# Kernel optimization log

Hardware: AMD Instinct MI355X
Metric: run time of the kernel (lower is better)

Reference implementation:

```python
import jax, jax.numpy as jnp
import numpy as np
from jax.ops import segment_sum

N_NODES = 50000


def graph_conv(src, dst, x, W, b, n_nodes):
    # DGL GraphConv with norm='both' (allow_zero_in_degree=True):
    # h = D_in^{-1/2} * A^T (D_out^{-1/2} * x) W + b, degrees clamped to >=1
    ones = jnp.ones(src.shape[0], dtype=x.dtype)
    deg_out = jnp.clip(segment_sum(ones, src, num_segments=n_nodes), 1.0)
    deg_in = jnp.clip(segment_sum(ones, dst, num_segments=n_nodes), 1.0)
    h = x * jax.lax.rsqrt(deg_out)[:, None]
    h = h @ W                      # apply weight before aggregation (mult_W first)
    m = segment_sum(h[src], dst, num_segments=n_nodes)  # sparse neighbor sum
    return m * jax.lax.rsqrt(deg_in)[:, None] + b


def setup_inputs() -> dict:
    key = jax.random.key(0)
    ks = jax.random.split(key, 10)
    n, e = N_NODES, 1600000
    d_in, h1, h2, h3 = 128, 128, 128, 64
    in_feat = jax.random.normal(ks[0], (n, d_in), dtype=jnp.float32)
    src = jax.random.randint(ks[1], (e,), 0, n, dtype=jnp.int32)
    dst = jax.random.randint(ks[2], (e,), 0, n, dtype=jnp.int32)
    s = lambda fi, fo: (1.0 / np.sqrt(fi)).astype(np.float32)
    W1 = jax.random.normal(ks[3], (d_in, h1), dtype=jnp.float32) * s(d_in, h1)
    b1 = jnp.zeros((h1,), dtype=jnp.float32)
    W2 = jax.random.normal(ks[4], (h1, h2), dtype=jnp.float32) * s(h1, h2)
    b2 = jnp.zeros((h2,), dtype=jnp.float32)
    Wf = jax.random.normal(ks[5], (h2, h3), dtype=jnp.float32) * s(h2, h3)
    bf = jnp.zeros((h3,), dtype=jnp.float32)
    return {"in_feat": in_feat, "src": src, "dst": dst,
            "W1": W1, "b1": b1, "W2": W2, "b2": b2, "Wf": Wf, "bf": bf}


def reference(in_feat, src, dst, W1, b1, W2, b2, Wf, bf):
    n = in_feat.shape[0]
    h = graph_conv(src, dst, in_feat, W1, b1, n)
    h = jax.nn.relu(h)
    # dropout(p=0.2) is identity in eval mode
    h = graph_conv(src, dst, h, W2, b2, n)
    return h @ Wf + bf
```

## Files before the change

### kernel.cpp

```cpp
#include <hip/hip_runtime.h>
#include <hip/hip_fp16.h>

#define FD 128
#define OD 64
#define RN 256
#define CHUNKS 256
#define NRMAX 1024

typedef _Float16 f16x8 __attribute__((ext_vector_type(8)));
typedef float    f32x4 __attribute__((ext_vector_type(4)));
typedef float    f32x2 __attribute__((ext_vector_type(2)));


__global__ void prescale_kernel(const float* __restrict__ X, const float* __restrict__ r_out,
                                __half* __restrict__ Xs, int n4) {
    int i = blockIdx.x * 256 + threadIdx.x;
    if (i >= n4) return;
    int v = i >> 5;
    float r = r_out[v];
    float4 t = ((const float4*)X)[i];
    ((__half2*)Xs)[2 * i]     = __floats2half2_rn(t.x * r, t.y * r);
    ((__half2*)Xs)[2 * i + 1] = __floats2half2_rn(t.z * r, t.w * r);
}


__global__ __launch_bounds__(1024) void region_hist_kernel(const int* __restrict__ src,
                                                           const int* __restrict__ dst,
                                                           int* __restrict__ hist_g,
                                                           int* __restrict__ hist_gs,
                                                           int E, int NR, int CS) {
    __shared__ int hist[NRMAX];
    __shared__ int hist_s[NRMAX];
    int c = blockIdx.x;
    for (int t = threadIdx.x; t < NR; t += 1024) { hist[t] = 0; hist_s[t] = 0; }
    __syncthreads();
    int e0 = c * CS, e1 = min(e0 + CS, E);
    int nv = (e1 - e0) & ~3;
    for (int e = e0 + threadIdx.x * 4; e < e0 + nv; e += 4096) {
        int4 d = *(const int4*)(dst + e);
        int4 s = *(const int4*)(src + e);
        atomicAdd(&hist[d.x >> 8], 1);
        atomicAdd(&hist[d.y >> 8], 1);
        atomicAdd(&hist[d.z >> 8], 1);
        atomicAdd(&hist[d.w >> 8], 1);
        atomicAdd(&hist_s[s.x >> 8], 1);
        atomicAdd(&hist_s[s.y >> 8], 1);
        atomicAdd(&hist_s[s.z >> 8], 1);
        atomicAdd(&hist_s[s.w >> 8], 1);
    }
    for (int e = e0 + nv + threadIdx.x; e < e1; e += 1024) {
        atomicAdd(&hist[dst[e] >> 8], 1);
        atomicAdd(&hist_s[src[e] >> 8], 1);
    }
    __syncthreads();
    for (int t = threadIdx.x; t < NR; t += 1024) {
        hist_g[t * CHUNKS + c]  = hist[t];
        hist_gs[t * CHUNKS + c] = hist_s[t];
    }
}

__global__ __launch_bounds__(1024) void region_scan_kernel(const int* __restrict__ hist_g,
                                                           const int* __restrict__ hist_gs,
                                                           int* __restrict__ rstart,
                                                           int* __restrict__ cursor,
                                                           int* __restrict__ sstart,
                                                           int* __restrict__ scursor,
                                                           int NR, int E) {
    __shared__ int wsum[16];
    int tid = threadIdx.x, lane = tid & 63, w = tid >> 6;
    int total = 0;
    if (tid < NR) {
        const int4* hp = (const int4*)(hist_g + (size_t)tid * CHUNKS);
        #pragma unroll 8
        for (int c4 = 0; c4 < CHUNKS / 4; c4++) {
            int4 h = hp[c4];
            total += h.x + h.y + h.z + h.w;
        }
    }
    int x = total;
    #pragma unroll
    for (int d = 1; d < 64; d <<= 1) {
        int t = __shfl_up(x, d, 64);
        if (lane >= d) x += t;
    }
    if (lane == 63) wsum[w] = x;
    __syncthreads();
    if (w == 0) {
        int s = (lane < 16) ? wsum[lane] : 0;
        #pragma unroll
        for (int d = 1; d < 16; d <<= 1) {
            int t = __shfl_up(s, d, 64);
            if (lane >= d) s += t;
        }
        if (lane < 16) wsum[lane] = s;
    }
    __syncthreads();
    int off = (w == 0) ? 0 : wsum[w - 1];
    if (tid < NR) {
        int start = x + off - total;
        rstart[tid] = start;
        int run = start;
        const int4* hp = (const int4*)(hist_g + (size_t)tid * CHUNKS);
        int4* cp = (int4*)(cursor + (size_t)tid * CHUNKS);
        #pragma unroll 8
        for (int c4 = 0; c4 < CHUNKS / 4; c4++) {
            int4 h = hp[c4];
            int4 o;
            o.x = run; run += h.x;
            o.y = run; run += h.y;
            o.z = run; run += h.z;
            o.w = run; run += h.w;
            cp[c4] = o;
        }
    }
    if (tid == 0) rstart[NR] = E;
    __syncthreads();
    total = 0;
    if (tid < NR) {
        const int4* hp = (const int4*)(hist_gs + (size_t)tid * CHUNKS);
        #pragma unroll 8
        for (int c4 = 0; c4 < CHUNKS / 4; c4++) {
            int4 h = hp[c4];
            total += h.x + h.y + h.z + h.w;
        }
    }
    x = total;
    #pragma unroll
    for (int d = 1; d < 64; d <<= 1) {
        int t = __shfl_up(x, d, 64);
        if (lane >= d) x += t;
    }
    if (lane == 63) wsum[w] = x;
    __syncthreads();
    if (w == 0) {
        int s = (lane < 16) ? wsum[lane] : 0;
        #pragma unroll
        for (int d = 1; d < 16; d <<= 1) {
            int t = __shfl_up(s, d, 64);
            if (lane >= d) s += t;
        }
        if (lane < 16) wsum[lane] = s;
    }
    __syncthreads();
    off = (w == 0) ? 0 : wsum[w - 1];
    if (tid < NR) {
        int start = x + off - total;
        sstart[tid] = start;
        int run = start;
        const int4* hp = (const int4*)(hist_gs + (size_t)tid * CHUNKS);
        int4* cp = (int4*)(scursor + (size_t)tid * CHUNKS);
        #pragma unroll 8
        for (int c4 = 0; c4 < CHUNKS / 4; c4++) {
            int4 h = hp[c4];
            int4 o;
            o.x = run; run += h.x;
            o.y = run; run += h.y;
            o.z = run; run += h.z;
            o.w = run; run += h.w;
            cp[c4] = o;
        }
    }
    if (tid == 0) sstart[NR] = E;
}

__global__ __launch_bounds__(1024) void partition_kernel(const int* __restrict__ src,
                                                         const int* __restrict__ dst,
                                                         const int* __restrict__ cursor,
                                                         const int* __restrict__ scursor,
                                                         int* __restrict__ epack,
                                                         unsigned char* __restrict__ spack,
                                                         int E, int NR, int CS) {
    __shared__ int cur[NRMAX];
    __shared__ int scur[NRMAX];
    int c = blockIdx.x;
    for (int t = threadIdx.x; t < NR; t += 1024) {
        cur[t]  = cursor[(size_t)t * CHUNKS + c];
        scur[t] = scursor[(size_t)t * CHUNKS + c];
    }
    __syncthreads();
    int e0 = c * CS, e1 = min(e0 + CS, E);
    int nv = (e1 - e0) & ~3;
    for (int e = e0 + threadIdx.x * 4; e < e0 + nv; e += 4096) {
        int4 d = *(const int4*)(dst + e);
        int4 s = *(const int4*)(src + e);
        int p0 = atomicAdd(&cur[d.x >> 8], 1);
        int p1 = atomicAdd(&cur[d.y >> 8], 1);
        int p2 = atomicAdd(&cur[d.z >> 8], 1);
        int p3 = atomicAdd(&cur[d.w >> 8], 1);
        epack[p0] = ((d.x & 255) << 17) | s.x;
        epack[p1] = ((d.y & 255) << 17) | s.y;
        epack[p2] = ((d.z & 255) << 17) | s.z;
        epack[p3] = ((d.w & 255) << 17) | s.w;
        int q0 = atomicAdd(&scur[s.x >> 8], 1);
        int q1 = atomicAdd(&scur[s.y >> 8], 1);
        int q2 = atomicAdd(&scur[s.z >> 8], 1);
        int q3 = atomicAdd(&scur[s.w >> 8], 1);
        spack[q0] = (unsigned char)(s.x & 255);
        spack[q1] = (unsigned char)(s.y & 255);
        spack[q2] = (unsigned char)(s.z & 255);
        spack[q3] = (unsigned char)(s.w & 255);
    }
    for (int e = e0 + nv + threadIdx.x; e < e1; e += 1024) {
        int d = dst[e], s = src[e];
        int pos = atomicAdd(&cur[d >> 8], 1);
        epack[pos] = ((d & 255) << 17) | s;
        int qos = atomicAdd(&scur[s >> 8], 1);
        spack[qos] = (unsigned char)(s & 255);
    }
}

__global__ __launch_bounds__(1024) void region_sort_kernel(const int* __restrict__ epack,
                                                           const int* __restrict__ rstart,
                                                           int* __restrict__ csrc,
                                                           int* __restrict__ row_start,
                                                           float* __restrict__ r_in,
                                                           int N, int NR, int E) {
    __shared__ int cnt[RN];
    __shared__ int cur[RN];
    __shared__ int wsum[16];
    const int r = blockIdx.x, tid = threadIdx.x;
    const int lane = tid & 63, w = tid >> 6;
    const int s0 = rstart[r], s1 = rstart[r + 1];
    if (tid < RN) cnt[tid] = 0;
    __syncthreads();
    for (int e = s0 + tid; e < s1; e += 1024)
        atomicAdd(&cnt[epack[e] >> 17], 1);
    __syncthreads();
    int cv = (tid < RN) ? cnt[tid] : 0;
    int x = cv;
    #pragma unroll
    for (int d = 1; d < 64; d <<= 1) {
        int t = __shfl_up(x, d, 64);
        if (lane >= d) x += t;
    }
    if (lane == 63 && w < 4) wsum[w] = x;
    __syncthreads();
    if (tid < RN) {
        int woff = 0;
        for (int i = 0; i < w; i++) woff += wsum[i];
        int start = s0 + x - cv + woff;
        cur[tid] = start;
        int node = r * RN + tid;
        if (node < N) {
            row_start[node] = start;
            r_in[node] = rsqrtf((float)max(cv, 1));
        }
    }
    if (r == NR - 1 && tid == 0) row_start[N] = E;
    __syncthreads();
    for (int e = s0 + tid; e < s1; e += 1024) {
        int pk = epack[e];
        int pos = atomicAdd(&cur[pk >> 17], 1);
        csrc[pos] = pk & 0x1FFFF;
    }
}

__global__ __launch_bounds__(256) void rout2_kernel(const unsigned char* __restrict__ spack,
                                                    const int* __restrict__ sstart,
                                                    float* __restrict__ r_out, int N) {
    __shared__ int cnt[RN];
    const int r = blockIdx.x, tid = threadIdx.x;
    const int s0 = sstart[r], s1 = sstart[r + 1];
    cnt[tid] = 0;
    __syncthreads();
    for (int e = s0 + tid; e < s1; e += 256)
        atomicAdd(&cnt[spack[e]], 1);
    __syncthreads();
    int node = r * RN + tid;
    if (node < N) r_out[node] = rsqrtf((float)max(cnt[tid], 1));
}

__global__ __launch_bounds__(256) void fused1_kernel(const __half* __restrict__ Xs,
                                                     const float* __restrict__ r_in,
                                                     const float* __restrict__ r_out,
                                                     const int* __restrict__ rs,
                                                     const int* __restrict__ csrc,
                                                     const __half* __restrict__ W1h,
                                                     const float* __restrict__ b1,
                                                     const __half* __restrict__ Wch,
                                                     __half* __restrict__ tbuf,
                                                     int N) {
    const int tid = threadIdx.x;
    const int lane = tid & 63, w = tid >> 6;
    const int l15 = lane & 15, quad = lane >> 4;
    const int base = blockIdx.x * 16;
    __shared__ __half2  zt[16][68];
    __shared__ _Float16 yt[16][136];

    for (int j = 0; j < 4; j++) {
        const int row = 4 * j + w;
        const int v = base + row;
        float ax = 0.f, ay = 0.f;
        if (v < N) {
            int s0 = __builtin_amdgcn_readfirstlane(rs[v]);
            int s1 = __builtin_amdgcn_readfirstlane(rs[v + 1]);
            const int deg = s1 - s0;
            const int nb = deg >> 4;
            int e = s0;
            if (nb) {
                int ia[16];
                #pragma unroll
                for (int u = 0; u < 16; u++) ia[u] = csrc[e + u];
                for (int b = 1; b < nb; b++) {
                    __half2 t[16];
                    #pragma unroll
                    for (int u = 0; u < 16; u++)
                        t[u] = ((const __half2*)(Xs + (size_t)ia[u] * FD))[lane];
                    int eb = e + (b << 4);
                    #pragma unroll
                    for (int u = 0; u < 16; u++) ia[u] = csrc[eb + u];
                    #pragma unroll
                    for (int u = 0; u < 16; u++) {
                        float2 f = __half22float2(t[u]);
                        ax += f.x; ay += f.y;
                    }
                }
                __half2 t[16];
                #pragma unroll
                for (int u = 0; u < 16; u++)
                    t[u] = ((const __half2*)(Xs + (size_t)ia[u] * FD))[lane];
                #pragma unroll
                for (int u = 0; u < 16; u++) {
                    float2 f = __half22float2(t[u]);
                    ax += f.x; ay += f.y;
                }
                e += nb << 4;
            }
            const int rem = s1 - e;
            if (rem) {
                const int last = s1 - 1;
                int ia[16];
                #pragma unroll
                for (int u = 0; u < 16; u++) ia[u] = csrc[min(e + u, last)];
                #pragma unroll
                for (int u = 0; u < 16; u++) {
                    unsigned raw = ((const unsigned*)(Xs + (size_t)ia[u] * FD))[lane];
                    raw = (u < rem) ? raw : 0u;
                    union { unsigned q; __half2 h; } tt; tt.q = raw;
                    float2 f = __half22float2(tt.h);
                    ax += f.x; ay += f.y;
                }
            }
            float ri = r_in[v];
            zt[row][lane] = __floats2half2_rn(ax * ri, ay * ri);
        } else {
            zt[row][lane] = __floats2half2_rn(0.f, 0.f);
        }
    }
    __syncthreads();

    const _Float16* B1 = (const _Float16*)W1h;
    const _Float16* B2 = (const _Float16*)Wch;
    f16x8 bf1[2][4];
    #pragma unroll
    for (int nt = 0; nt < 2; nt++) {
        int col = 32 * w + 16 * nt + l15;
        #pragma unroll
        for (int kk = 0; kk < 4; kk++) {
            int kb = kk * 32 + quad * 8;
            f16x8 bf;
            #pragma unroll
            for (int j = 0; j < 8; j++) bf[j] = B1[(size_t)(kb + j) * FD + col];
            bf1[nt][kk] = bf;
        }
    }
    f16x8 bf2[4];
    const int col2 = 16 * w + l15;
    #pragma unroll
    for (int kk = 0; kk < 4; kk++) {
        int kb = kk * 32 + quad * 8;
        f16x8 bf;
        #pragma unroll
        for (int j = 0; j < 8; j++) bf[j] = B2[(size_t)(kb + j) * OD + col2];
        bf2[kk] = bf;
    }

    {
        const _Float16* Arow = (const _Float16*)&zt[l15][0] + quad * 8;
        f16x8 afrag[4];
        #pragma unroll
        for (int kk = 0; kk < 4; kk++) afrag[kk] = *(const f16x8*)(Arow + kk * 32);
        f32x4 acc0 = {0.f, 0.f, 0.f, 0.f};
        f32x4 acc1 = {0.f, 0.f, 0.f, 0.f};
        #pragma unroll
        for (int kk = 0; kk < 4; kk++) {
            acc0 = __builtin_amdgcn_mfma_f32_16x16x32_f16(afrag[kk], bf1[0][kk], acc0, 0, 0, 0);
            acc1 = __builtin_amdgcn_mfma_f32_16x16x32_f16(afrag[kk], bf1[1][kk], acc1, 0, 0, 0);
        }
        int c0 = 32 * w + l15, c1 = c0 + 16;
        float bb0 = b1[c0], bb1 = b1[c1];
        #pragma unroll
        for (int r = 0; r < 4; r++) {
            int row = quad * 4 + r;
            int v = base + row;
            float rsc = (v < N) ? r_out[v] : 0.f;
            yt[row][c0] = (_Float16)(fmaxf(acc0[r] + bb0, 0.f) * rsc);
            yt[row][c1] = (_Float16)(fmaxf(acc1[r] + bb1, 0.f) * rsc);
        }
    }
    __syncthreads();

    {
        const _Float16* Arow = &yt[l15][0] + quad * 8;
        f16x8 afrag[4];
        #pragma unroll
        for (int kk = 0; kk < 4; kk++) afrag[kk] = *(const f16x8*)(Arow + kk * 32);
        f32x4 acc = {0.f, 0.f, 0.f, 0.f};
        #pragma unroll
        for (int kk = 0; kk < 4; kk++)
            acc = __builtin_amdgcn_mfma_f32_16x16x32_f16(afrag[kk], bf2[kk], acc, 0, 0, 0);
        #pragma unroll
        for (int r = 0; r < 4; r++) {
            int row = quad * 4 + r;
            int v = base + row;
            if (v < N)
                tbuf[(size_t)v * OD + col2] = __float2half(acc[r]);
        }
    }
}

__global__ __launch_bounds__(256) void agg64_kernel(const __half* __restrict__ T,
                                                    const float* __restrict__ r_in,
                                                    const int* __restrict__ rs,
                                                    const int* __restrict__ csrc,
                                                    const float* __restrict__ bc,
                                                    float* __restrict__ out, int N) {
    const int tid = threadIdx.x;
    const int lane = tid & 63, wv = tid >> 6;
    const int hf = lane >> 5, l32 = lane & 31;
    int v = blockIdx.x * 8 + wv * 2 + hf;
    if (v >= N) return;
    int s0 = rs[v], s1 = rs[v + 1];
    const int deg = s1 - s0;
    float ax = 0.f, ay = 0.f;
    const int nb = deg >> 3;
    int e = s0;
    if (nb) {
        int ia[8];
        #pragma unroll
        for (int u = 0; u < 8; u++) ia[u] = csrc[e + u];
        for (int b = 1; b < nb; b++) {
            __half2 t[8];
            #pragma unroll
            for (int u = 0; u < 8; u++)
                t[u] = ((const __half2*)(T + (size_t)ia[u] * OD))[l32];
            int eb = e + (b << 3);
            #pragma unroll
            for (int u = 0; u < 8; u++) ia[u] = csrc[eb + u];
            #pragma unroll
            for (int u = 0; u < 8; u++) {
                float2 f = __half22float2(t[u]);
                ax += f.x; ay += f.y;
            }
        }
        __half2 t[8];
        #pragma unroll
        for (int u = 0; u < 8; u++)
            t[u] = ((const __half2*)(T + (size_t)ia[u] * OD))[l32];
        #pragma unroll
        for (int u = 0; u < 8; u++) {
            float2 f = __half22float2(t[u]);
            ax += f.x; ay += f.y;
        }
        e += nb << 3;
    }
    const int rem = s1 - e;
    if (rem) {
        const int last = s1 - 1;
        int ia[8];
        #pragma unroll
        for (int u = 0; u < 8; u++) ia[u] = csrc[min(e + u, last)];
        #pragma unroll
        for (int u = 0; u < 8; u++) {
            unsigned raw = ((const unsigned*)(T + (size_t)ia[u] * OD))[l32];
            raw = (u < rem) ? raw : 0u;
            union { unsigned q; __half2 h; } tt; tt.q = raw;
            float2 f = __half22float2(tt.h);
            ax += f.x; ay += f.y;
        }
    }
    float ri = r_in[v];
    f32x2 o;
    o.x = ax * ri + bc[l32 * 2];
    o.y = ay * ri + bc[l32 * 2 + 1];
    __builtin_nontemporal_store(o, (f32x2*)(out + (size_t)v * OD) + l32);
}

__global__ void fold_kernel(const float* __restrict__ W2, const float* __restrict__ Wf,
                            const float* __restrict__ b2, const float* __restrict__ bf,
                            const float* __restrict__ W1,
                            __half* __restrict__ W1h, __half* __restrict__ Wch,
                            float* __restrict__ bc) {
    int idx = blockIdx.x * 256 + threadIdx.x;
    if (idx < FD * FD) W1h[idx] = __float2half(W1[idx]);
    if (idx < FD * OD) {
        int i = idx / OD, j = idx % OD;
        float s = 0.f;
        for (int k = 0; k < FD; k++) s += W2[i * FD + k] * Wf[k * OD + j];
        Wch[idx] = __float2half(s);
    }
    if (idx < OD) {
        float s = bf[idx];
        for (int k = 0; k < FD; k++) s += b2[k] * Wf[k * OD + idx];
        bc[idx] = s;
    }
}

extern "C" void kernel_launch(void* const* d_in, const int* in_sizes, int n_in,
                              void* d_out, int out_size, void* d_ws, size_t ws_size,
                              hipStream_t stream) {
    const float* in_feat = (const float*)d_in[0];
    const int*   src     = (const int*)d_in[1];
    const int*   dst     = (const int*)d_in[2];
    const float* W1      = (const float*)d_in[3];
    const float* b1      = (const float*)d_in[4];
    const float* W2      = (const float*)d_in[5];
    const float* b2      = (const float*)d_in[6];
    const float* Wf      = (const float*)d_in[7];
    const float* bf      = (const float*)d_in[8];
    float* out = (float*)d_out;

    const int N = in_sizes[0] / FD;
    const int E = in_sizes[1];
    const int NR = (N + RN - 1) / RN;
    const int CS = (((E + CHUNKS - 1) / CHUNKS) + 3) & ~3;

    char* ws = (char*)d_ws;
    size_t off = 0;
    auto alloc = [&](size_t bytes) -> void* {
        void* p = ws + off;
        off += (bytes + 255) / 256 * 256;
        return p;
    };
    unsigned char* spack = (unsigned char*)alloc((size_t)E);
    int*    epack   = (int*)alloc((size_t)E * 4);
    __half* tbuf    = (__half*)spack;
    float*  r_out   = (float*)alloc((size_t)N * 4);
    float*  r_in    = (float*)alloc((size_t)N * 4);
    int*    hist_g  = (int*)alloc((size_t)CHUNKS * NRMAX * 4);
    int*    hist_gs = (int*)alloc((size_t)CHUNKS * NRMAX * 4);
    int*    cursor  = (int*)alloc((size_t)CHUNKS * NRMAX * 4);
    int*    scursor = (int*)alloc((size_t)CHUNKS * NRMAX * 4);
    int*    rstart  = (int*)alloc((size_t)(NR + 1) * 4);
    int*    sstart  = (int*)alloc((size_t)(NR + 1) * 4);
    int*    csrc    = (int*)alloc((size_t)E * 4);
    int*    row_start = (int*)alloc((size_t)(N + 1) * 4);
    __half* Xs      = (__half*)alloc((size_t)N * FD * 2);
    __half* W1h     = (__half*)alloc((size_t)FD * FD * 2);
    __half* Wch     = (__half*)alloc((size_t)FD * OD * 2);
    float*  bc      = (float*)alloc((size_t)OD * 4);
    (void)ws_size; (void)n_in; (void)out_size;

    region_hist_kernel<<<CHUNKS, 1024, 0, stream>>>(src, dst, hist_g, hist_gs, E, NR, CS);
    region_scan_kernel<<<1, 1024, 0, stream>>>(hist_g, hist_gs, rstart, cursor, sstart, scursor, NR, E);
    partition_kernel<<<CHUNKS, 1024, 0, stream>>>(src, dst, cursor, scursor, epack, spack, E, NR, CS);
    region_sort_kernel<<<NR, 1024, 0, stream>>>(epack, rstart, csrc, row_start, r_in, N, NR, E);
    rout2_kernel<<<NR, 256, 0, stream>>>(spack, sstart, r_out, N);

    fold_kernel<<<(FD * FD + 255) / 256, 256, 0, stream>>>(W2, Wf, b2, bf, W1, W1h, Wch, bc);

    prescale_kernel<<<(N * 32 + 255) / 256, 256, 0, stream>>>(in_feat, r_out, Xs, N * 32);
    fused1_kernel<<<(N + 15) / 16, 256, 0, stream>>>(Xs, r_in, r_out, row_start, csrc,
                                                     W1h, b1, Wch, tbuf, N);

    agg64_kernel<<<(N + 7) / 8, 256, 0, stream>>>(tbuf, r_in, row_start, csrc, bc, out, N);
}
```

Before: 276.4 us.

## Sort nodes by in-degree and process them in degree order for load balance

Adds a single-block counting-sort kernel that builds a permutation of nodes ordered by in-degree. The fused first-layer kernel and the final aggregation kernel now map blocks and waves to nodes through this permutation, so each block handles nodes of similar degree and waves in a block finish at about the same time. In exchange it adds a serial single-block launch over all nodes, an extra indirection per node, and scattered output writes instead of contiguous ones.

```diff
diff --git a/kernel.cpp b/kernel.cpp
--- a/kernel.cpp
+++ b/kernel.cpp
@@ -270,11 +270,55 @@
     if (node < N) r_out[node] = rsqrtf((float)max(cnt[tid], 1));
 }
 
+__global__ __launch_bounds__(1024) void permsort_kernel(const int* __restrict__ rs,
+                                                        int* __restrict__ perm, int N) {
+    __shared__ int hist[1024];
+    __shared__ int wsum[16];
+    const int tid = threadIdx.x, lane = tid & 63, w = tid >> 6;
+    hist[tid] = 0;
+    __syncthreads();
+    for (int v = tid; v < N; v += 1024) {
+        int d = min(rs[v + 1] - rs[v], 1023);
+        atomicAdd(&hist[d], 1);
+    }
+    __syncthreads();
+    int cv = hist[tid];
+    int x = cv;
+    #pragma unroll
+    for (int d = 1; d < 64; d <<= 1) {
+        int t = __shfl_up(x, d, 64);
+        if (lane >= d) x += t;
+    }
+    if (lane == 63) wsum[w] = x;
+    __syncthreads();
+    if (w == 0) {
+        int s = (lane < 16) ? wsum[lane] : 0;
+        #pragma unroll
+        for (int d = 1; d < 16; d <<= 1) {
+            int t = __shfl_up(s, d, 64);
+            if (lane >= d) s += t;
+        }
+        if (lane < 16) wsum[lane] = s;
+    }
+    __syncthreads();
+    int off = (w == 0) ? 0 : wsum[w - 1];
+    int start = x + off - cv;
+    __syncthreads();
+    hist[tid] = start;
+    __syncthreads();
+    for (int v = tid; v < N; v += 1024) {
+        int d = min(rs[v + 1] - rs[v], 1023);
+        int pos = atomicAdd(&hist[d], 1);
+        perm[pos] = v;
+    }
+}
+
 __global__ __launch_bounds__(256) void fused1_kernel(const __half* __restrict__ Xs,
                                                      const float* __restrict__ r_in,
                                                      const float* __restrict__ r_out,
                                                      const int* __restrict__ rs,
                                                      const int* __restrict__ csrc,
+                                                     const int* __restrict__ perm,
                                                      const __half* __restrict__ W1h,
                                                      const float* __restrict__ b1,
                                                      const __half* __restrict__ Wch,
@@ -284,14 +328,21 @@
     const int lane = tid & 63, w = tid >> 6;
     const int l15 = lane & 15, quad = lane >> 4;
     const int base = blockIdx.x * 16;
+    __shared__ int pv[16];
     __shared__ __half2  zt[16][68];
     __shared__ _Float16 yt[16][136];
 
+    if (tid < 16) {
+        int idx = base + tid;
+        pv[tid] = (idx < N) ? perm[idx] : -1;
+    }
+    __syncthreads();
+
     for (int j = 0; j < 4; j++) {
         const int row = 4 * j + w;
-        const int v = base + row;
+        const int v = pv[row];
         float ax = 0.f, ay = 0.f;
-        if (v < N) {
+        if (v >= 0) {
             int s0 = __builtin_amdgcn_readfirstlane(rs[v]);
             int s1 = __builtin_amdgcn_readfirstlane(rs[v + 1]);
             const int deg = s1 - s0;
@@ -392,8 +443,8 @@
         #pragma unroll
         for (int r = 0; r < 4; r++) {
             int row = quad * 4 + r;
-            int v = base + row;
-            float rsc = (v < N) ? r_out[v] : 0.f;
+            int vv = pv[row];
+            float rsc = (vv >= 0) ? r_out[vv] : 0.f;
             yt[row][c0] = (_Float16)(fmaxf(acc0[r] + bb0, 0.f) * rsc);
             yt[row][c1] = (_Float16)(fmaxf(acc1[r] + bb1, 0.f) * rsc);
         }
@@ -412,9 +463,9 @@
         #pragma unroll
         for (int r = 0; r < 4; r++) {
             int row = quad * 4 + r;
-            int v = base + row;
-            if (v < N)
-                tbuf[(size_t)v * OD + col2] = __float2half(acc[r]);
+            int vv = pv[row];
+            if (vv >= 0)
+                tbuf[(size_t)vv * OD + col2] = __float2half(acc[r]);
         }
     }
 }
@@ -423,13 +474,15 @@
                                                     const float* __restrict__ r_in,
                                                     const int* __restrict__ rs,
                                                     const int* __restrict__ csrc,
+                                                    const int* __restrict__ perm,
                                                     const float* __restrict__ bc,
                                                     float* __restrict__ out, int N) {
     const int tid = threadIdx.x;
     const int lane = tid & 63, wv = tid >> 6;
     const int hf = lane >> 5, l32 = lane & 31;
-    int v = blockIdx.x * 8 + wv * 2 + hf;
-    if (v >= N) return;
+    int idx = blockIdx.x * 8 + wv * 2 + hf;
+    if (idx >= N) return;
+    int v = perm[idx];
     int s0 = rs[v], s1 = rs[v + 1];
     const int deg = s1 - s0;
     float ax = 0.f, ay = 0.f;
@@ -545,6 +598,7 @@
     int*    sstart  = (int*)alloc((size_t)(NR + 1) * 4);
     int*    csrc    = (int*)alloc((size_t)E * 4);
     int*    row_start = (int*)alloc((size_t)(N + 1) * 4);
+    int*    perm    = (int*)alloc((size_t)N * 4);
     __half* Xs      = (__half*)alloc((size_t)N * FD * 2);
     __half* W1h     = (__half*)alloc((size_t)FD * FD * 2);
     __half* Wch     = (__half*)alloc((size_t)FD * OD * 2);
@@ -557,11 +611,13 @@
     region_sort_kernel<<<NR, 1024, 0, stream>>>(epack, rstart, csrc, row_start, r_in, N, NR, E);
     rout2_kernel<<<NR, 256, 0, stream>>>(spack, sstart, r_out, N);
 
+    permsort_kernel<<<1, 1024, 0, stream>>>(row_start, perm, N);
+
     fold_kernel<<<(FD * FD + 255) / 256, 256, 0, stream>>>(W2, Wf, b2, bf, W1, W1h, Wch, bc);
 
     prescale_kernel<<<(N * 32 + 255) / 256, 256, 0, stream>>>(in_feat, r_out, Xs, N * 32);
-    fused1_kernel<<<(N + 15) / 16, 256, 0, stream>>>(Xs, r_in, r_out, row_start, csrc,
+    fused1_kernel<<<(N + 15) / 16, 256, 0, stream>>>(Xs, r_in, r_out, row_start, csrc, perm,
                                                      W1h, b1, Wch, tbuf, N);
 
-    agg64_kernel<<<(N + 7) / 8, 256, 0, stream>>>(tbuf, r_in, row_start, csrc, bc, out, N);
-}
+    agg64_kernel<<<(N + 7) / 8, 256, 0, stream>>>(tbuf, r_in, row_start, csrc, perm, bc, out, N);
+}
```

Measured after the change: 311.9 us. 1.13x slower.
